# Kernel tuning notes

Measured on AMD Instinct MI355X. Metric: run time of the kernel, lower is better.

The kernel has to match this reference:

```python
import jax, jax.numpy as jnp
import numpy as np

N_NODES = 100000
N_EDGES = 1200000
N_GRAPHS = 500
IN_DIM, HID, OUT = 128, 64, 16


def setup_inputs() -> dict:
    key = jax.random.key(0)
    ks = jax.random.split(key, 10)
    x = jax.random.normal(ks[0], (N_NODES, IN_DIM), dtype=jnp.float32)
    edge_index = jax.random.randint(ks[1], (2, N_EDGES), 0, N_NODES, dtype=jnp.int64)
    batch = jnp.sort(jax.random.randint(ks[2], (N_NODES,), 0, N_GRAPHS, dtype=jnp.int64))
    # Glorot-style init for GCN linear weights, zero bias (PyG default)
    def glorot(k, fan_in, fan_out):
        s = jnp.sqrt(6.0 / (fan_in + fan_out))
        return jax.random.uniform(k, (fan_in, fan_out), jnp.float32, -s, s)
    W1 = glorot(ks[3], IN_DIM, HID); b1 = jnp.zeros((HID,), jnp.float32)
    W2 = glorot(ks[4], HID, HID);    b2 = jnp.zeros((HID,), jnp.float32)
    W3 = glorot(ks[5], HID, OUT);    b3 = jnp.zeros((OUT,), jnp.float32)
    return {"x": x, "edge_index": edge_index, "batch": batch,
            "W1": W1, "b1": b1, "W2": W2, "b2": b2, "W3": W3, "b3": b3}


def gcn_conv(x, src, dst, deg_inv_sqrt, W, b, n_nodes):
    # PyG GCNConv: h = x @ W; aggregate with sym-normalized A+I; add bias.
    h = x @ W  # [N, F_out]
    norm = deg_inv_sqrt[src] * deg_inv_sqrt[dst]            # [E]
    msg = h[src] * norm[:, None]                            # gather + scale
    agg = jax.ops.segment_sum(msg, dst, num_segments=n_nodes)
    agg = agg + h * (deg_inv_sqrt * deg_inv_sqrt)[:, None]  # self-loop term
    return agg + b


def reference(x, edge_index, batch, W1, b1, W2, b2, W3, b3):
    n = x.shape[0]
    src, dst = edge_index[0], edge_index[1]
    # degree of A + I (count incoming edges at dst, plus self-loop)
    deg = 1.0 + jax.ops.segment_sum(jnp.ones_like(src, dtype=x.dtype), dst, num_segments=n)
    dis = deg ** -0.5  # deg >= 1 so always finite
    h = gcn_conv(x, src, dst, dis, W1, b1, n)
    h = jax.nn.relu(h)
    h = gcn_conv(h, src, dst, dis, W2, b2, n)
    h = jax.nn.relu(h)
    h = gcn_conv(h, src, dst, dis, W3, b3, n)
    # global_mean_pool over graph ids
    sums = jax.ops.segment_sum(h, batch, num_segments=N_GRAPHS)
    counts = jax.ops.segment_sum(jnp.ones((n,), h.dtype), batch, num_segments=N_GRAPHS)
    return sums / jnp.clip(counts, 1.0)[:, None]
```

## Files before the change

kernel.cpp:

```cpp
#include <hip/hip_runtime.h>
#include <hip/hip_bf16.h>
#include <hip/hip_fp16.h>

#define IN_DIM 128
#define HID    64
#define OUTF   16
#define NGRAPH 500

#define CE    2048
#define NRNG  16
#define CAP   256
#define NG    32
#define RSZ   6272

__device__ __forceinline__ uint2 f4_to_h4(float4 a) {
    __half2 lo = __floats2half2_rn(a.x, a.y);
    __half2 hi = __floats2half2_rn(a.z, a.w);
    uint2 r;
    r.x = *(unsigned*)&lo;
    r.y = *(unsigned*)&hi;
    return r;
}
__device__ __forceinline__ float4 h4_to_f4(uint2 q) {
    __half2 a = *(__half2*)&q.x, b = *(__half2*)&q.y;
    float2 fa = __half22float2(a), fb = __half22float2(b);
    return make_float4(fa.x, fa.y, fb.x, fb.y);
}
__device__ __forceinline__ void h8_to_f8(uint4 p, float4& f0, float4& f1) {
    __half2 a = *(__half2*)&p.x, b = *(__half2*)&p.y;
    __half2 c = *(__half2*)&p.z, d = *(__half2*)&p.w;
    float2 fa = __half22float2(a), fb = __half22float2(b);
    float2 fc = __half22float2(c), fd = __half22float2(d);
    f0 = make_float4(fa.x, fa.y, fb.x, fb.y);
    f1 = make_float4(fc.x, fc.y, fd.x, fd.y);
}

template<int K>
__global__ __launch_bounds__(256, 4) void gemm64_kernel(const float* __restrict__ X,
                                                        const float* __restrict__ W,
                                                        __half* __restrict__ Hh, int N) {
    constexpr int BK = 64;
    constexpr int PAD = 4;
    constexpr int LDX = BK + PAD;
    constexpr int K4 = K / 4;
    __shared__ float sX[64 * LDX];
    __shared__ float sW[BK * 64];
    const int tid = threadIdx.x;
    const int row0 = blockIdx.x * 64;
    const int tc = tid & 15;
    const int tr = tid >> 4;

    const float4* W4 = (const float4*)W;
    const float4* X4 = (const float4*)X;
    float4* sW4 = (float4*)sW;

    float4 acc0 = {0,0,0,0}, acc1 = {0,0,0,0}, acc2 = {0,0,0,0}, acc3 = {0,0,0,0};

    for (int k0 = 0; k0 < K; k0 += BK) {
        for (int i = tid; i < BK * 16; i += 256) sW4[i] = W4[k0 * 16 + i];
        for (int i = tid; i < 64 * (BK / 4); i += 256) {
            int r = i >> 4, kk = i & 15;
            int gr = row0 + r;
            float4 v = {0.f, 0.f, 0.f, 0.f};
            if (gr < N) v = X4[(long long)gr * K4 + (k0 >> 2) + kk];
            *(float4*)&sX[r * LDX + kk * 4] = v;
        }
        __syncthreads();

        const float* sX0 = &sX[(tr * 4) * LDX];
#pragma unroll 4
        for (int k = 0; k < BK; k += 4) {
            float4 x0 = *(const float4*)&sX0[k];
            float4 x1 = *(const float4*)&sX0[LDX + k];
            float4 x2 = *(const float4*)&sX0[2 * LDX + k];
            float4 x3 = *(const float4*)&sX0[3 * LDX + k];
            float4 w0 = sW4[(k + 0) * 16 + tc];
            float4 w1 = sW4[(k + 1) * 16 + tc];
            float4 w2 = sW4[(k + 2) * 16 + tc];
            float4 w3 = sW4[(k + 3) * 16 + tc];
            acc0.x += x0.x * w0.x; acc0.y += x0.x * w0.y; acc0.z += x0.x * w0.z; acc0.w += x0.x * w0.w;
            acc1.x += x1.x * w0.x; acc1.y += x1.x * w0.y; acc1.z += x1.x * w0.z; acc1.w += x1.x * w0.w;
            acc2.x += x2.x * w0.x; acc2.y += x2.x * w0.y; acc2.z += x2.x * w0.z; acc2.w += x2.x * w0.w;
            acc3.x += x3.x * w0.x; acc3.y += x3.x * w0.y; acc3.z += x3.x * w0.z; acc3.w += x3.x * w0.w;
            acc0.x += x0.y * w1.x; acc0.y += x0.y * w1.y; acc0.z += x0.y * w1.z; acc0.w += x0.y * w1.w;
            acc1.x += x1.y * w1.x; acc1.y += x1.y * w1.y; acc1.z += x1.y * w1.z; acc1.w += x1.y * w1.w;
            acc2.x += x2.y * w1.x; acc2.y += x2.y * w1.y; acc2.z += x2.y * w1.z; acc2.w += x2.y * w1.w;
            acc3.x += x3.y * w1.x; acc3.y += x3.y * w1.y; acc3.z += x3.y * w1.z; acc3.w += x3.y * w1.w;
            acc0.x += x0.z * w2.x; acc0.y += x0.z * w2.y; acc0.z += x0.z * w2.z; acc0.w += x0.z * w2.w;
            acc1.x += x1.z * w2.x; acc1.y += x1.z * w2.y; acc1.z += x1.z * w2.z; acc1.w += x1.z * w2.w;
            acc2.x += x2.z * w2.x; acc2.y += x2.z * w2.y; acc2.z += x2.z * w2.z; acc2.w += x2.z * w2.w;
            acc3.x += x3.z * w2.x; acc3.y += x3.z * w2.y; acc3.z += x3.z * w2.z; acc3.w += x3.z * w2.w;
            acc0.x += x0.w * w3.x; acc0.y += x0.w * w3.y; acc0.z += x0.w * w3.z; acc0.w += x0.w * w3.w;
            acc1.x += x1.w * w3.x; acc1.y += x1.w * w3.y; acc1.z += x1.w * w3.z; acc1.w += x1.w * w3.w;
            acc2.x += x2.w * w3.x; acc2.y += x2.w * w3.y; acc2.z += x2.w * w3.z; acc2.w += x2.w * w3.w;
            acc3.x += x3.w * w3.x; acc3.y += x3.w * w3.y; acc3.z += x3.w * w3.z; acc3.w += x3.w * w3.w;
        }
        __syncthreads();
    }

    uint2* Hh2 = (uint2*)Hh;
    int r0 = row0 + tr * 4;
    if (r0 + 0 < N) Hh2[(long long)(r0 + 0) * 16 + tc] = f4_to_h4(acc0);
    if (r0 + 1 < N) Hh2[(long long)(r0 + 1) * 16 + tc] = f4_to_h4(acc1);
    if (r0 + 2 < N) Hh2[(long long)(r0 + 2) * 16 + tc] = f4_to_h4(acc2);
    if (r0 + 3 < N) Hh2[(long long)(r0 + 3) * 16 + tc] = f4_to_h4(acc3);
}

template<int K, int F>
__global__ __launch_bounds__(256) void gemm_kernel(const float* __restrict__ X,
                                                   const float* __restrict__ W,
                                                   __half* __restrict__ Hh, int N) {
    constexpr int C4 = F / 4;
    constexpr int ROWS = 256 / C4;
    constexpr int K4 = K / 4;
    constexpr int LDX4 = K4 + 1;
    __shared__ float4 sW[K * C4];
    __shared__ float4 sX4[ROWS * LDX4];
    const int tid = threadIdx.x;
    const float4* W4 = (const float4*)W;
    for (int i = tid; i < K * C4; i += 256) sW[i] = W4[i];
    const int row0 = blockIdx.x * ROWS;
    const float4* X4 = (const float4*)X;
    for (int i = tid; i < ROWS * K4; i += 256) {
        int r = i / K4, kk = i - r * K4;
        int gr = row0 + r;
        float4 z = {0.f, 0.f, 0.f, 0.f};
        sX4[r * LDX4 + kk] = (gr < N) ? X4[(long long)gr * K4 + kk] : z;
    }
    __syncthreads();
    const int r = tid / C4, c4 = tid - (tid / C4) * C4;
    const float* sXr = (const float*)&sX4[r * LDX4];
    float4 acc = {0.f, 0.f, 0.f, 0.f};
#pragma unroll
    for (int k = 0; k < K; ++k) {
        float xv = sXr[k];
        float4 wv = sW[k * C4 + c4];
        acc.x += xv * wv.x; acc.y += xv * wv.y;
        acc.z += xv * wv.z; acc.w += xv * wv.w;
    }
    const int gr = row0 + r;
    if (gr < N) ((uint2*)Hh)[(long long)gr * C4 + c4] = f4_to_h4(acc);
}

__global__ __launch_bounds__(256) void part_kernel(const int* __restrict__ src,
                                                   const int* __restrict__ dst,
                                                   uint2* __restrict__ seg,
                                                   int* __restrict__ segcnt,
                                                   int E, int rangeSize) {
    __shared__ uint2 sSeg[NRNG][CAP];
    __shared__ int sCnt[NRNG];
    const int tid = threadIdx.x;
    if (tid < NRNG) sCnt[tid] = 0;
    __syncthreads();
    const int base = blockIdx.x * CE + tid;
    int d[8], s[8];
#pragma unroll
    for (int k = 0; k < 8; ++k) {
        int e = base + k * 256;
        d[k] = (e < E) ? dst[e] : -1;
        s[k] = (e < E) ? src[e] : 0;
    }
#pragma unroll
    for (int k = 0; k < 8; ++k) {
        if (d[k] >= 0) {
            int r = d[k] / rangeSize;
            int li = atomicAdd(&sCnt[r], 1);
            if (li < CAP) sSeg[r][li] = make_uint2((unsigned)s[k], (unsigned)d[k]);
        }
    }
    __syncthreads();
    for (int r = 0; r < NRNG; ++r) {
        int n = sCnt[r] < CAP ? sCnt[r] : CAP;
        uint2* out = seg + ((size_t)(blockIdx.x * NRNG + r)) * CAP;
        for (int i = tid; i < n; i += 256) out[i] = sSeg[r][i];
        if (tid == 0) segcnt[blockIdx.x * NRNG + r] = n;
    }
}

__global__ __launch_bounds__(256) void count_kernel(const uint2* __restrict__ seg,
                                                    const int* __restrict__ segcnt,
                                                    int* __restrict__ cnt,
                                                    int N, int rangeSize, int nchunks) {
    __shared__ int hist[RSZ];
    const int r = blockIdx.x & (NRNG - 1);
    const int g = blockIdx.x / NRNG;
    const int cpg = (nchunks + NG - 1) / NG;
    const int c0 = g * cpg;
    const int c1 = (c0 + cpg < nchunks) ? c0 + cpg : nchunks;
    for (int i = threadIdx.x; i < rangeSize; i += 256) hist[i] = 0;
    __syncthreads();
    const int base = r * rangeSize;
    for (int c = c0; c < c1; ++c) {
        const int si = c * NRNG + r;
        const int n = segcnt[si];
        const uint2* s = seg + (size_t)si * CAP;
        for (int i = threadIdx.x; i < n; i += 256)
            atomicAdd(&hist[(int)s[i].y - base], 1);
    }
    __syncthreads();
    const int lim = (base + rangeSize <= N) ? rangeSize : (N - base);
    for (int i = threadIdx.x; i < lim; i += 256)
        cnt[(size_t)g * N + base + i] = hist[i];
}

__global__ __launch_bounds__(1024) void scan1_kernel(int* __restrict__ cnt,
                                                     int* __restrict__ rowptr,
                                                     int* __restrict__ aux,
                                                     float* __restrict__ dis,
                                                     float* __restrict__ pool0, int N) {
    if (blockIdx.x == 0) {
        for (int i = threadIdx.x; i < NGRAPH * OUTF + NGRAPH; i += 1024) pool0[i] = 0.f;
    }
    __shared__ int s[1024];
    int i = blockIdx.x * 1024 + threadIdx.x;
    int v = 0;
    if (i < N) {
        int run = 0;
#pragma unroll
        for (int g = 0; g < NG; ++g) {
            const size_t idx = (size_t)g * N + i;
            int c = cnt[idx];
            cnt[idx] = run;
            run += c;
        }
        v = run;
        dis[i] = rsqrtf(1.0f + (float)v);
    }
    s[threadIdx.x] = v;
    __syncthreads();
    for (int off = 1; off < 1024; off <<= 1) {
        int t = (threadIdx.x >= off) ? s[threadIdx.x - off] : 0;
        __syncthreads();
        s[threadIdx.x] += t;
        __syncthreads();
    }
    if (i < N) rowptr[i] = s[threadIdx.x] - v;
    if (threadIdx.x == 1023) aux[blockIdx.x] = s[1023];
}

__global__ __launch_bounds__(1024) void scan3_kernel(int* __restrict__ rowptr,
                                                     const int* __restrict__ aux,
                                                     int N, int nb) {
    __shared__ int s[128];
    const int t = threadIdx.x;
    if (t < 128) s[t] = (t < nb) ? aux[t] : 0;
    __syncthreads();
    for (int off = 1; off < 128; off <<= 1) {
        int v = (t >= off && t < 128) ? s[t - off] : 0;
        __syncthreads();
        if (t < 128) s[t] += v;
        __syncthreads();
    }
    int add = (blockIdx.x == 0) ? 0 : s[blockIdx.x - 1];
    int i = blockIdx.x * 1024 + t;
    if (i < N) rowptr[i] += add;
}

__global__ __launch_bounds__(256) void scatter_kernel(const uint2* __restrict__ seg,
                                                      const int* __restrict__ segcnt,
                                                      const int* __restrict__ cntp,
                                                      const int* __restrict__ rowptr,
                                                      int* __restrict__ csr_src,
                                                      int N, int rangeSize, int nchunks) {
    __shared__ int hist[RSZ];
    const int r = blockIdx.x & (NRNG - 1);
    const int g = blockIdx.x / NRNG;
    const int cpg = (nchunks + NG - 1) / NG;
    const int c0 = g * cpg;
    const int c1 = (c0 + cpg < nchunks) ? c0 + cpg : nchunks;
    for (int i = threadIdx.x; i < rangeSize; i += 256) hist[i] = 0;
    __syncthreads();
    const int base = r * rangeSize;
    for (int c = c0; c < c1; ++c) {
        const int si = c * NRNG + r;
        const int n = segcnt[si];
        const uint2* s = seg + (size_t)si * CAP;
        for (int i = threadIdx.x; i < n; i += 256) {
            uint2 v = s[i];
            const int d = (int)v.y;
            const int rank = atomicAdd(&hist[d - base], 1);
            csr_src[rowptr[d] + cntp[(size_t)g * N + d] + rank] = (int)v.x;
        }
    }
}

template<bool RELU>
__global__ __launch_bounds__(256) void agg64_kernel(const __half* __restrict__ Hh,
                                                    const int* __restrict__ rowptr,
                                                    const int* __restrict__ csr_src,
                                                    const float* __restrict__ dis,
                                                    const float4* __restrict__ b4,
                                                    float4* __restrict__ out4, int N, int E) {
    const int tid = threadIdx.x;
    const int lane = tid & 63;
    const int node = blockIdx.x * 16 + (tid >> 6) * 4 + (lane >> 4);
    const int g2 = (lane >> 3) & 1;
    const int c = lane & 7;
    if (node >= N) return;
    const uint4* Hh4 = (const uint4*)Hh;
    float dd = dis[node];
    int i0 = rowptr[node];
    int i1 = (node + 1 < N) ? rowptr[node + 1] : E;
    float4 a0 = {0.f, 0.f, 0.f, 0.f}, a1 = {0.f, 0.f, 0.f, 0.f};
    int i = i0 + g2;
    int iB = i + 2;
    int sA = (i < i1) ? csr_src[i] : 0;
    int sB = (iB < i1) ? csr_src[iB] : 0;
    uint4 pA = make_uint4(0u, 0u, 0u, 0u);
    float wA = 0.f;
    if (i < i1) {
        pA = Hh4[(long long)sA * 8 + c];
        wA = dis[sA] * dd;
    }
    while (i < i1) {
        const int iC = i + 4;
        int sC = (iC < i1) ? csr_src[iC] : 0;
        uint4 pB = Hh4[(long long)sB * 8 + c];
        float wB = (iB < i1) ? dis[sB] * dd : 0.f;
        float4 v0, v1;
        h8_to_f8(pA, v0, v1);
        a0.x += v0.x * wA; a0.y += v0.y * wA; a0.z += v0.z * wA; a0.w += v0.w * wA;
        a1.x += v1.x * wA; a1.y += v1.y * wA; a1.z += v1.z * wA; a1.w += v1.w * wA;
        i = iB; iB = iC; sA = sB; sB = sC; pA = pB; wA = wB;
    }
    a0.x += __shfl_xor(a0.x, 8); a0.y += __shfl_xor(a0.y, 8);
    a0.z += __shfl_xor(a0.z, 8); a0.w += __shfl_xor(a0.w, 8);
    a1.x += __shfl_xor(a1.x, 8); a1.y += __shfl_xor(a1.y, 8);
    a1.z += __shfl_xor(a1.z, 8); a1.w += __shfl_xor(a1.w, 8);
    if (g2 == 0) {
        float sl = dd * dd;
        uint4 ps = Hh4[(long long)node * 8 + c];
        float4 h0, h1;
        h8_to_f8(ps, h0, h1);
        float4 bb0 = b4[2 * c], bb1 = b4[2 * c + 1];
        a0.x += h0.x * sl + bb0.x; a0.y += h0.y * sl + bb0.y;
        a0.z += h0.z * sl + bb0.z; a0.w += h0.w * sl + bb0.w;
        a1.x += h1.x * sl + bb1.x; a1.y += h1.y * sl + bb1.y;
        a1.z += h1.z * sl + bb1.z; a1.w += h1.w * sl + bb1.w;
        if (RELU) {
            a0.x = fmaxf(a0.x, 0.f); a0.y = fmaxf(a0.y, 0.f);
            a0.z = fmaxf(a0.z, 0.f); a0.w = fmaxf(a0.w, 0.f);
            a1.x = fmaxf(a1.x, 0.f); a1.y = fmaxf(a1.y, 0.f);
            a1.z = fmaxf(a1.z, 0.f); a1.w = fmaxf(a1.w, 0.f);
        }
        out4[(long long)node * 16 + 2 * c] = a0;
        out4[(long long)node * 16 + 2 * c + 1] = a1;
    }
}

template<bool RELU>
__global__ __launch_bounds__(256) void agg16_kernel(const __half* __restrict__ Hh,
                                                    const int* __restrict__ rowptr,
                                                    const int* __restrict__ csr_src,
                                                    const float* __restrict__ dis,
                                                    const float4* __restrict__ b4,
                                                    float4* __restrict__ out4, int N, int E) {
    const int tid = threadIdx.x;
    const int lane = tid & 63;
    const int node = blockIdx.x * 32 + (tid >> 6) * 8 + (lane >> 3);
    const int g2 = (lane >> 2) & 1;
    const int c = lane & 3;
    if (node >= N) return;
    const uint2* Hh2 = (const uint2*)Hh;
    float dd = dis[node];
    int i0 = rowptr[node];
    int i1 = (node + 1 < N) ? rowptr[node + 1] : E;
    float4 acc = {0.f, 0.f, 0.f, 0.f};
    int i = i0 + g2;
    int iB = i + 2;
    int sA = (i < i1) ? csr_src[i] : 0;
    int sB = (iB < i1) ? csr_src[iB] : 0;
    uint2 pA = make_uint2(0u, 0u);
    float wA = 0.f;
    if (i < i1) {
        pA = Hh2[(long long)sA * 4 + c];
        wA = dis[sA] * dd;
    }
    while (i < i1) {
        const int iC = i + 4;
        int sC = (iC < i1) ? csr_src[iC] : 0;
        uint2 pB = Hh2[(long long)sB * 4 + c];
        float wB = (iB < i1) ? dis[sB] * dd : 0.f;
        float4 v = h4_to_f4(pA);
        acc.x += v.x * wA; acc.y += v.y * wA;
        acc.z += v.z * wA; acc.w += v.w * wA;
        i = iB; iB = iC; sA = sB; sB = sC; pA = pB; wA = wB;
    }
    acc.x += __shfl_xor(acc.x, 4);
    acc.y += __shfl_xor(acc.y, 4);
    acc.z += __shfl_xor(acc.z, 4);
    acc.w += __shfl_xor(acc.w, 4);
    if (g2 == 0) {
        float4 h = h4_to_f4(Hh2[(long long)node * 4 + c]);
        float sl = dd * dd;
        float4 bb = b4[c];
        acc.x += h.x * sl + bb.x; acc.y += h.y * sl + bb.y;
        acc.z += h.z * sl + bb.z; acc.w += h.w * sl + bb.w;
        if (RELU) {
            acc.x = fmaxf(acc.x, 0.f); acc.y = fmaxf(acc.y, 0.f);
            acc.z = fmaxf(acc.z, 0.f); acc.w = fmaxf(acc.w, 0.f);
        }
        out4[(long long)node * 4 + c] = acc;
    }
}

__global__ __launch_bounds__(256) void pool_kernel(const float4* __restrict__ H4,
                                                   const int* __restrict__ batch,
                                                   float* __restrict__ sums,
                                                   float* __restrict__ cnts, int N) {
    __shared__ float sBin[16][16];
    __shared__ float sCnt[16];
    const int t = threadIdx.x;
    sBin[t >> 4][t & 15] = 0.f;
    if (t < 16) sCnt[t] = 0.f;
    __syncthreads();
    const int n0 = blockIdx.x * 256;
    const int g0 = batch[n0];
    const int nl = t >> 2;
    const int f4 = t & 3;
    float4 acc = {0.f, 0.f, 0.f, 0.f};
    float cnt = 0.f;
    int curli = -1;
    for (int j = 0; j < 4; ++j) {
        int node = n0 + nl * 4 + j;
        if (node >= N) break;
        int li = batch[node] - g0;
        if (li != curli) {
            if (curli >= 0) {
                if (curli < 16) {
                    float* bp = &sBin[curli][f4 * 4];
                    atomicAdd(bp + 0, acc.x); atomicAdd(bp + 1, acc.y);
                    atomicAdd(bp + 2, acc.z); atomicAdd(bp + 3, acc.w);
                    if (f4 == 0) atomicAdd(&sCnt[curli], cnt);
                } else {
                    float* gp = &sums[(g0 + curli) * OUTF + f4 * 4];
                    atomicAdd(gp + 0, acc.x); atomicAdd(gp + 1, acc.y);
                    atomicAdd(gp + 2, acc.z); atomicAdd(gp + 3, acc.w);
                    if (f4 == 0) atomicAdd(&cnts[g0 + curli], cnt);
                }
            }
            acc.x = acc.y = acc.z = acc.w = 0.f; cnt = 0.f; curli = li;
        }
        float4 v = H4[(long long)node * 4 + f4];
        acc.x += v.x; acc.y += v.y; acc.z += v.z; acc.w += v.w;
        cnt += 1.f;
    }
    if (curli >= 0) {
        if (curli < 16) {
            float* bp = &sBin[curli][f4 * 4];
            atomicAdd(bp + 0, acc.x); atomicAdd(bp + 1, acc.y);
            atomicAdd(bp + 2, acc.z); atomicAdd(bp + 3, acc.w);
            if (f4 == 0) atomicAdd(&sCnt[curli], cnt);
        } else {
            float* gp = &sums[(g0 + curli) * OUTF + f4 * 4];
            atomicAdd(gp + 0, acc.x); atomicAdd(gp + 1, acc.y);
            atomicAdd(gp + 2, acc.z); atomicAdd(gp + 3, acc.w);
            if (f4 == 0) atomicAdd(&cnts[g0 + curli], cnt);
        }
    }
    __syncthreads();
    int bg = t >> 4, bf = t & 15;
    int g = g0 + bg;
    if (g < NGRAPH) {
        float v = sBin[bg][bf];
        if (v != 0.f) atomicAdd(&sums[g * OUTF + bf], v);
        if (bf == 0) {
            float c = sCnt[bg];
            if (c != 0.f) atomicAdd(&cnts[g], c);
        }
    }
}

__global__ void divide_kernel(const float* __restrict__ sums, const float* __restrict__ counts,
                              float* __restrict__ out) {
    int i = blockIdx.x * blockDim.x + threadIdx.x;
    if (i < NGRAPH * OUTF) out[i] = sums[i] / fmaxf(counts[i >> 4], 1.0f);
}

extern "C" void kernel_launch(void* const* d_in, const int* in_sizes, int n_in,
                              void* d_out, int out_size, void* d_ws, size_t ws_size,
                              hipStream_t stream) {
    const float* x     = (const float*)d_in[0];
    const int*   ei    = (const int*)d_in[1];
    const int*   batch = (const int*)d_in[2];
    const float* W1 = (const float*)d_in[3];
    const float* b1 = (const float*)d_in[4];
    const float* W2 = (const float*)d_in[5];
    const float* b2 = (const float*)d_in[6];
    const float* W3 = (const float*)d_in[7];
    const float* b3 = (const float*)d_in[8];
    float* out = (float*)d_out;

    const int N = in_sizes[2];
    const int E = in_sizes[1] / 2;
    const int* src = ei;
    const int* dst = ei + E;

    const int nchunks = (E + CE - 1) / CE;
    const int NGB = NG * NRNG;

    float*    ws      = (float*)d_ws;
    float*    dis     = ws;
    float*    bufA    = dis + N;
    float*    bufB    = bufA + (size_t)N * HID;
    float*    sums    = bufB + (size_t)N * HID;
    float*    cnts    = sums + NGRAPH * OUTF;
    int*      rowptr  = (int*)(cnts + NGRAPH);
    int*      csr_src = rowptr + N;
    int*      segcnt  = csr_src + E;
    int*      aux     = segcnt + nchunks * NRNG;
    uint2*    seg     = (uint2*)bufB;
    int*      cntmat  = (int*)bufA;
    __half*   Hh      = (__half*)bufA;

    const int B = 256;
    const int nb = (N + 1023) / 1024;
    const int rangeSize = (N + NRNG - 1) / NRNG;

    part_kernel<<<nchunks, B, 0, stream>>>(src, dst, seg, segcnt, E, rangeSize);
    count_kernel<<<NGB, B, 0, stream>>>(seg, segcnt, cntmat, N, rangeSize, nchunks);
    scan1_kernel<<<nb, 1024, 0, stream>>>(cntmat, rowptr, aux, dis, sums, N);
    scan3_kernel<<<nb, 1024, 0, stream>>>(rowptr, aux, N, nb);
    scatter_kernel<<<NGB, B, 0, stream>>>(seg, segcnt, cntmat, rowptr, csr_src, N, rangeSize, nchunks);

    gemm64_kernel<IN_DIM><<<(N + 63) / 64, B, 0, stream>>>(x, W1, Hh, N);
    agg64_kernel<true><<<(N + 15) / 16, B, 0, stream>>>(Hh, rowptr, csr_src,
                                                        dis, (const float4*)b1, (float4*)bufB, N, E);

    gemm64_kernel<HID><<<(N + 63) / 64, B, 0, stream>>>(bufB, W2, Hh, N);
    agg64_kernel<true><<<(N + 15) / 16, B, 0, stream>>>(Hh, rowptr, csr_src,
                                                        dis, (const float4*)b2, (float4*)bufB, N, E);

    gemm_kernel<HID, OUTF><<<(N + 63) / 64, B, 0, stream>>>(bufB, W3, Hh, N);
    agg16_kernel<false><<<(N + 31) / 32, B, 0, stream>>>(Hh, rowptr, csr_src,
                                                         dis, (const float4*)b3, (float4*)bufB, N, E);

    pool_kernel<<<(N + 255) / 256, B, 0, stream>>>((const float4*)bufB, batch, sums, cnts, N);
    divide_kernel<<<(NGRAPH * OUTF + B - 1) / B, B, 0, stream>>>(sums, cnts, out);
}
```

Baseline: 289.5 us.

## Use fp16 MFMA for the three GEMMs and store hidden activations in fp16

Replaces the scalar FP32 register-tiled GEMM kernels with a single templated kernel that stages X and a transposed W in LDS as fp16 and computes with 16x16x32 f16 MFMA instructions, writing the fp16 result through LDS as coalesced 16-byte stores. The aggregation kernel now writes its ReLU output as fp16 instead of fp32, so the next GEMM reads half the bytes. This cuts ALU time and memory traffic for the dense stages. The cost is an extra rounding of the layer inputs to fp16, which adds some numerical error.

```diff
diff --git a/kernel.cpp b/kernel.cpp
--- a/kernel.cpp
+++ b/kernel.cpp
@@ -12,6 +12,9 @@
 #define CAP   256
 #define NG    32
 #define RSZ   6272
+
+typedef _Float16 f16x8 __attribute__((ext_vector_type(8)));
+typedef float    f32x4v __attribute__((ext_vector_type(4)));
 
 __device__ __forceinline__ uint2 f4_to_h4(float4 a) {
     __half2 lo = __floats2half2_rn(a.x, a.y);
@@ -35,111 +38,89 @@
     f1 = make_float4(fc.x, fc.y, fd.x, fd.y);
 }
 
-template<int K>
-__global__ __launch_bounds__(256, 4) void gemm64_kernel(const float* __restrict__ X,
-                                                        const float* __restrict__ W,
-                                                        __half* __restrict__ Hh, int N) {
-    constexpr int BK = 64;
-    constexpr int PAD = 4;
-    constexpr int LDX = BK + PAD;
-    constexpr int K4 = K / 4;
-    __shared__ float sX[64 * LDX];
-    __shared__ float sW[BK * 64];
+template<int K, int F, bool INF16>
+__global__ __launch_bounds__(256, 4) void mfma_gemm_kernel(const void* __restrict__ Xv,
+                                                           const float* __restrict__ W,
+                                                           __half* __restrict__ Hh, int N) {
+    constexpr int Kp = K + 8;
+    constexpr int CT = F / 16;
+    __shared__ _Float16 sA[64 * Kp];
+    __shared__ _Float16 sBt[F * Kp];
     const int tid = threadIdx.x;
     const int row0 = blockIdx.x * 64;
-    const int tc = tid & 15;
-    const int tr = tid >> 4;
-
-    const float4* W4 = (const float4*)W;
-    const float4* X4 = (const float4*)X;
-    float4* sW4 = (float4*)sW;
-
-    float4 acc0 = {0,0,0,0}, acc1 = {0,0,0,0}, acc2 = {0,0,0,0}, acc3 = {0,0,0,0};
-
-    for (int k0 = 0; k0 < K; k0 += BK) {
-        for (int i = tid; i < BK * 16; i += 256) sW4[i] = W4[k0 * 16 + i];
-        for (int i = tid; i < 64 * (BK / 4); i += 256) {
-            int r = i >> 4, kk = i & 15;
+
+    if (INF16) {
+        const uint4* X8 = (const uint4*)Xv;
+        constexpr int Q = K / 8;
+        for (int i = tid; i < 64 * Q; i += 256) {
+            int r = i / Q, q = i - r * Q;
+            int gr = row0 + r;
+            uint4 v = make_uint4(0u, 0u, 0u, 0u);
+            if (gr < N) v = X8[(size_t)gr * Q + q];
+            *(uint4*)&sA[r * Kp + q * 8] = v;
+        }
+    } else {
+        const float4* X4 = (const float4*)Xv;
+        constexpr int Q = K / 4;
+        for (int i = tid; i < 64 * Q; i += 256) {
+            int r = i / Q, q = i - r * Q;
             int gr = row0 + r;
             float4 v = {0.f, 0.f, 0.f, 0.f};
-            if (gr < N) v = X4[(long long)gr * K4 + (k0 >> 2) + kk];
-            *(float4*)&sX[r * LDX + kk * 4] = v;
-        }
-        __syncthreads();
-
-        const float* sX0 = &sX[(tr * 4) * LDX];
-#pragma unroll 4
-        for (int k = 0; k < BK; k += 4) {
-            float4 x0 = *(const float4*)&sX0[k];
-            float4 x1 = *(const float4*)&sX0[LDX + k];
-            float4 x2 = *(const float4*)&sX0[2 * LDX + k];
-            float4 x3 = *(const float4*)&sX0[3 * LDX + k];
-            float4 w0 = sW4[(k + 0) * 16 + tc];
-            float4 w1 = sW4[(k + 1) * 16 + tc];
-            float4 w2 = sW4[(k + 2) * 16 + tc];
-            float4 w3 = sW4[(k + 3) * 16 + tc];
-            acc0.x += x0.x * w0.x; acc0.y += x0.x * w0.y; acc0.z += x0.x * w0.z; acc0.w += x0.x * w0.w;
-            acc1.x += x1.x * w0.x; acc1.y += x1.x * w0.y; acc1.z += x1.x * w0.z; acc1.w += x1.x * w0.w;
-            acc2.x += x2.x * w0.x; acc2.y += x2.x * w0.y; acc2.z += x2.x * w0.z; acc2.w += x2.x * w0.w;
-            acc3.x += x3.x * w0.x; acc3.y += x3.x * w0.y; acc3.z += x3.x * w0.z; acc3.w += x3.x * w0.w;
-            acc0.x += x0.y * w1.x; acc0.y += x0.y * w1.y; acc0.z += x0.y * w1.z; acc0.w += x0.y * w1.w;
-            acc1.x += x1.y * w1.x; acc1.y += x1.y * w1.y; acc1.z += x1.y * w1.z; acc1.w += x1.y * w1.w;
-            acc2.x += x2.y * w1.x; acc2.y += x2.y * w1.y; acc2.z += x2.y * w1.z; acc2.w += x2.y * w1.w;
-            acc3.x += x3.y * w1.x; acc3.y += x3.y * w1.y; acc3.z += x3.y * w1.z; acc3.w += x3.y * w1.w;
-            acc0.x += x0.z * w2.x; acc0.y += x0.z * w2.y; acc0.z += x0.z * w2.z; acc0.w += x0.z * w2.w;
-            acc1.x += x1.z * w2.x; acc1.y += x1.z * w2.y; acc1.z += x1.z * w2.z; acc1.w += x1.z * w2.w;
-            acc2.x += x2.z * w2.x; acc2.y += x2.z * w2.y; acc2.z += x2.z * w2.z; acc2.w += x2.z * w2.w;
-            acc3.x += x3.z * w2.x; acc3.y += x3.z * w2.y; acc3.z += x3.z * w2.z; acc3.w += x3.z * w2.w;
-            acc0.x += x0.w * w3.x; acc0.y += x0.w * w3.y; acc0.z += x0.w * w3.z; acc0.w += x0.w * w3.w;
-            acc1.x += x1.w * w3.x; acc1.y += x1.w * w3.y; acc1.z += x1.w * w3.z; acc1.w += x1.w * w3.w;
-            acc2.x += x2.w * w3.x; acc2.y += x2.w * w3.y; acc2.z += x2.w * w3.z; acc2.w += x2.w * w3.w;
-            acc3.x += x3.w * w3.x; acc3.y += x3.w * w3.y; acc3.z += x3.w * w3.z; acc3.w += x3.w * w3.w;
-        }
-        __syncthreads();
-    }
-
-    uint2* Hh2 = (uint2*)Hh;
-    int r0 = row0 + tr * 4;
-    if (r0 + 0 < N) Hh2[(long long)(r0 + 0) * 16 + tc] = f4_to_h4(acc0);
-    if (r0 + 1 < N) Hh2[(long long)(r0 + 1) * 16 + tc] = f4_to_h4(acc1);
-    if (r0 + 2 < N) Hh2[(long long)(r0 + 2) * 16 + tc] = f4_to_h4(acc2);
-    if (r0 + 3 < N) Hh2[(long long)(r0 + 3) * 16 + tc] = f4_to_h4(acc3);
-}
-
-template<int K, int F>
-__global__ __launch_bounds__(256) void gemm_kernel(const float* __restrict__ X,
-                                                   const float* __restrict__ W,
-                                                   __half* __restrict__ Hh, int N) {
-    constexpr int C4 = F / 4;
-    constexpr int ROWS = 256 / C4;
-    constexpr int K4 = K / 4;
-    constexpr int LDX4 = K4 + 1;
-    __shared__ float4 sW[K * C4];
-    __shared__ float4 sX4[ROWS * LDX4];
-    const int tid = threadIdx.x;
-    const float4* W4 = (const float4*)W;
-    for (int i = tid; i < K * C4; i += 256) sW[i] = W4[i];
-    const int row0 = blockIdx.x * ROWS;
-    const float4* X4 = (const float4*)X;
-    for (int i = tid; i < ROWS * K4; i += 256) {
-        int r = i / K4, kk = i - r * K4;
+            if (gr < N) v = X4[(size_t)gr * Q + q];
+            *(uint2*)&sA[r * Kp + q * 4] = f4_to_h4(v);
+        }
+    }
+    {
+        const float4* W4 = (const float4*)W;
+        for (int i = tid; i < K * (F / 4); i += 256) {
+            int k = i / (F / 4), c4 = i - k * (F / 4);
+            float4 v = W4[i];
+            sBt[(c4 * 4 + 0) * Kp + k] = (_Float16)v.x;
+            sBt[(c4 * 4 + 1) * Kp + k] = (_Float16)v.y;
+            sBt[(c4 * 4 + 2) * Kp + k] = (_Float16)v.z;
+            sBt[(c4 * 4 + 3) * Kp + k] = (_Float16)v.w;
+        }
+    }
+    __syncthreads();
+
+    const int w = tid >> 6;
+    const int l = tid & 63;
+    const int m16 = l & 15;
+    const int kg = l >> 4;
+
+    f32x4v acc[CT];
+#pragma unroll
+    for (int t = 0; t < CT; ++t) acc[t] = (f32x4v){0.f, 0.f, 0.f, 0.f};
+
+    const _Float16* pa = &sA[(w * 16 + m16) * Kp + kg * 8];
+#pragma unroll
+    for (int k0 = 0; k0 < K; k0 += 32) {
+        f16x8 af = *(const f16x8*)(pa + k0);
+#pragma unroll
+        for (int t = 0; t < CT; ++t) {
+            f16x8 bf = *(const f16x8*)&sBt[(t * 16 + m16) * Kp + k0 + kg * 8];
+            acc[t] = __builtin_amdgcn_mfma_f32_16x16x32_f16(af, bf, acc[t], 0, 0, 0);
+        }
+    }
+    __syncthreads();
+    _Float16* sOut = sA;
+#pragma unroll
+    for (int t = 0; t < CT; ++t) {
+#pragma unroll
+        for (int r = 0; r < 4; ++r) {
+            int m = w * 16 + kg * 4 + r;
+            int n = t * 16 + m16;
+            sOut[m * F + n] = (_Float16)acc[t][r];
+        }
+    }
+    __syncthreads();
+    constexpr int U4 = (F * 2) / 16;
+    uint4* Ho = (uint4*)Hh;
+    for (int i = tid; i < 64 * U4; i += 256) {
+        int r = i / U4, q = i - r * U4;
         int gr = row0 + r;
-        float4 z = {0.f, 0.f, 0.f, 0.f};
-        sX4[r * LDX4 + kk] = (gr < N) ? X4[(long long)gr * K4 + kk] : z;
-    }
-    __syncthreads();
-    const int r = tid / C4, c4 = tid - (tid / C4) * C4;
-    const float* sXr = (const float*)&sX4[r * LDX4];
-    float4 acc = {0.f, 0.f, 0.f, 0.f};
-#pragma unroll
-    for (int k = 0; k < K; ++k) {
-        float xv = sXr[k];
-        float4 wv = sW[k * C4 + c4];
-        acc.x += xv * wv.x; acc.y += xv * wv.y;
-        acc.z += xv * wv.z; acc.w += xv * wv.w;
-    }
-    const int gr = row0 + r;
-    if (gr < N) ((uint2*)Hh)[(long long)gr * C4 + c4] = f4_to_h4(acc);
+        if (gr < N) Ho[(size_t)gr * U4 + q] = *(uint4*)&sOut[r * F + q * 8];
+    }
 }
 
 __global__ __launch_bounds__(256) void part_kernel(const int* __restrict__ src,
@@ -284,13 +265,12 @@
     }
 }
 
-template<bool RELU>
 __global__ __launch_bounds__(256) void agg64_kernel(const __half* __restrict__ Hh,
                                                     const int* __restrict__ rowptr,
                                                     const int* __restrict__ csr_src,
                                                     const float* __restrict__ dis,
                                                     const float4* __restrict__ b4,
-                                                    float4* __restrict__ out4, int N, int E) {
+                                                    uint4* __restrict__ outh, int N, int E) {
     const int tid = threadIdx.x;
     const int lane = tid & 63;
     const int node = blockIdx.x * 16 + (tid >> 6) * 4 + (lane >> 4);
@@ -337,14 +317,12 @@
         a0.z += h0.z * sl + bb0.z; a0.w += h0.w * sl + bb0.w;
         a1.x += h1.x * sl + bb1.x; a1.y += h1.y * sl + bb1.y;
         a1.z += h1.z * sl + bb1.z; a1.w += h1.w * sl + bb1.w;
-        if (RELU) {
-            a0.x = fmaxf(a0.x, 0.f); a0.y = fmaxf(a0.y, 0.f);
-            a0.z = fmaxf(a0.z, 0.f); a0.w = fmaxf(a0.w, 0.f);
-            a1.x = fmaxf(a1.x, 0.f); a1.y = fmaxf(a1.y, 0.f);
-            a1.z = fmaxf(a1.z, 0.f); a1.w = fmaxf(a1.w, 0.f);
-        }
-        out4[(long long)node * 16 + 2 * c] = a0;
-        out4[(long long)node * 16 + 2 * c + 1] = a1;
+        a0.x = fmaxf(a0.x, 0.f); a0.y = fmaxf(a0.y, 0.f);
+        a0.z = fmaxf(a0.z, 0.f); a0.w = fmaxf(a0.w, 0.f);
+        a1.x = fmaxf(a1.x, 0.f); a1.y = fmaxf(a1.y, 0.f);
+        a1.z = fmaxf(a1.z, 0.f); a1.w = fmaxf(a1.w, 0.f);
+        uint2 lo = f4_to_h4(a0), hi = f4_to_h4(a1);
+        outh[(long long)node * 8 + c] = make_uint4(lo.x, lo.y, hi.x, hi.y);
     }
 }
 
@@ -511,7 +489,8 @@
     int*      aux     = segcnt + nchunks * NRNG;
     uint2*    seg     = (uint2*)bufB;
     int*      cntmat  = (int*)bufA;
-    __half*   Hh      = (__half*)bufA;
+    __half*   HhA     = (__half*)bufA;
+    __half*   HhB     = (__half*)bufB;
 
     const int B = 256;
     const int nb = (N + 1023) / 1024;
@@ -523,16 +502,18 @@
     scan3_kernel<<<nb, 1024, 0, stream>>>(rowptr, aux, N, nb);
     scatter_kernel<<<NGB, B, 0, stream>>>(seg, segcnt, cntmat, rowptr, csr_src, N, rangeSize, nchunks);
 
-    gemm64_kernel<IN_DIM><<<(N + 63) / 64, B, 0, stream>>>(x, W1, Hh, N);
-    agg64_kernel<true><<<(N + 15) / 16, B, 0, stream>>>(Hh, rowptr, csr_src,
-                                                        dis, (const float4*)b1, (float4*)bufB, N, E);
-
-    gemm64_kernel<HID><<<(N + 63) / 64, B, 0, stream>>>(bufB, W2, Hh, N);
-    agg64_kernel<true><<<(N + 15) / 16, B, 0, stream>>>(Hh, rowptr, csr_src,
-                                                        dis, (const float4*)b2, (float4*)bufB, N, E);
-
-    gemm_kernel<HID, OUTF><<<(N + 63) / 64, B, 0, stream>>>(bufB, W3, Hh, N);
-    agg16_kernel<false><<<(N + 31) / 32, B, 0, stream>>>(Hh, rowptr, csr_src,
+    const int gb = (N + 63) / 64;
+
+    mfma_gemm_kernel<IN_DIM, HID, false><<<gb, B, 0, stream>>>(x, W1, HhA, N);
+    agg64_kernel<<<(N + 15) / 16, B, 0, stream>>>(HhA, rowptr, csr_src,
+                                                  dis, (const float4*)b1, (uint4*)HhB, N, E);
+
+    mfma_gemm_kernel<HID, HID, true><<<gb, B, 0, stream>>>(HhB, W2, HhA, N);
+    agg64_kernel<<<(N + 15) / 16, B, 0, stream>>>(HhA, rowptr, csr_src,
+                                                  dis, (const float4*)b2, (uint4*)HhB, N, E);
+
+    mfma_gemm_kernel<HID, OUTF, true><<<gb, B, 0, stream>>>(HhB, W3, HhA, N);
+    agg16_kernel<false><<<(N + 31) / 32, B, 0, stream>>>(HhA, rowptr, csr_src,
                                                          dis, (const float4*)b3, (float4*)bufB, N, E);
 
     pool_kernel<<<(N + 255) / 256, B, 0, stream>>>((const float4*)bufB, batch, sums, cnts, N);
```

Measured after the change: 268.4 us. -7.3%, faster.
